# Performance work log

Measured on AMD Instinct MI355X. Metric: run time of the kernel, lower is better.

Reference implementation:

```python
import jax, jax.numpy as jnp
import numpy as np

D_MODEL = 1024
N_HEADS = 16
HEAD_DIM = D_MODEL // N_HEADS
SCALE = HEAD_DIM ** -0.5
MASK_FILL = -10000.0


def setup_inputs() -> dict:
    key = jax.random.key(0)
    ks = jax.random.split(key, 12)
    B, L, D = 2, 2048, D_MODEL
    inv = 1.0 / np.sqrt(D)
    inp = {
        "query": jax.random.normal(ks[0], (B, L, D), jnp.float32),
        "key": jax.random.normal(ks[1], (B, L, D), jnp.float32),
        "value": jax.random.normal(ks[2], (B, L, D), jnp.float32),
        "Wq": jax.random.normal(ks[3], (D, D), jnp.float32) * inv,
        "bq": jnp.zeros((D,), jnp.float32),
        "Wk": jax.random.normal(ks[4], (D, D), jnp.float32) * inv,
        "bk": jnp.zeros((D,), jnp.float32),
        "Wv": jax.random.normal(ks[5], (D, D), jnp.float32) * inv,
        "bv": jnp.zeros((D,), jnp.float32),
        "Wo": jax.random.normal(ks[6], (D, D), jnp.float32) * inv,
        "bo": jnp.zeros((D,), jnp.float32),
        "valid_mask": jax.random.randint(ks[7], (B, L), 0, 2).astype(jnp.bool_),
    }
    return inp


def reference(query, key, value, Wq, bq, Wk, bk, Wv, bv, Wo, bo, valid_mask):
    B, Lq, D = query.shape
    Lk = key.shape[1]
    H, HD = N_HEADS, HEAD_DIM
    # torch.nn.Linear: y = x @ W.T + b
    Q = (query @ Wq.T + bq).reshape(B, Lq, H, HD).transpose(0, 2, 1, 3)  # [B,H,Lq,HD]
    K = (key @ Wk.T + bk).reshape(B, Lk, H, HD).transpose(0, 2, 1, 3)    # [B,H,Lk,HD]
    V = (value @ Wv.T + bv).reshape(B, Lk, H, HD).transpose(0, 2, 1, 3)  # [B,H,Lk,HD]
    scores = jnp.einsum("bhqd,bhkd->bhqk", Q, K) * SCALE
    scores = jnp.where(valid_mask[:, None, None, :], scores, MASK_FILL)
    weights = jax.nn.softmax(scores, axis=-1)  # dropout is identity at inference
    out = jnp.einsum("bhqk,bhkd->bhqd", weights, V)
    out = out.transpose(0, 2, 1, 3).reshape(B, Lq, D)
    out = out @ Wo.T + bo
    # zero rows of fully-invalid batches
    gate = jnp.any(valid_mask, axis=1).astype(out.dtype)[:, None, None]
    return out * gate
```

## Files before the change

kernel.cpp:

```cpp
#include <hip/hip_runtime.h>
#include <hip/hip_bf16.h>

typedef __hip_bfloat16 bf16;
typedef __attribute__((ext_vector_type(8))) short s8v;
typedef __attribute__((ext_vector_type(4))) float f4v;

#define LOG2E 1.44269504088896340736f
#define CSCALE (0.125f * LOG2E)
#define MASK_B2 (-14426.950408889634f)
#define NEG_BIG (-30000.0f)

#define BB 2
#define LL 2048
#define DD 1024
#define HH 16
#define HD 64
#define MTOT 4096
#define PER_T 4194304

struct alignas(8) B4 { bf16 v[4]; };

__device__ __forceinline__ void async_cp16(const bf16* g, bf16* l) {
    __builtin_amdgcn_global_load_lds(
        (const __attribute__((address_space(1))) void*)g,
        (__attribute__((address_space(3))) void*)l, 16, 0, 0);
}

struct CvtArgs {
    const float* src[7];
    bf16* dst[7];
    int n[7];
};

__global__ __launch_bounds__(256) void cvt_kernel(CvtArgs args) {
    const int which = blockIdx.y;
    const float* __restrict__ src = args.src[which];
    bf16* __restrict__ dst = args.dst[which];
    const int n4 = args.n[which] >> 2;
    const int stride = gridDim.x * 256;
    for (int i = blockIdx.x * 256 + threadIdx.x; i < n4; i += stride) {
        const float4 f = ((const float4*)src)[i];
        B4 o;
        o.v[0] = __float2bfloat16(f.x);
        o.v[1] = __float2bfloat16(f.y);
        o.v[2] = __float2bfloat16(f.z);
        o.v[3] = __float2bfloat16(f.w);
        ((B4*)dst)[i] = o;
    }
}

struct QkvArgs {
    const bf16* A[3];
    const bf16* W[3];
    const float* bias[3];
    bf16* out[3];
};

template <int FUSED, int SWAP>
__device__ __forceinline__ void gemm_body(const bf16* __restrict__ A,
                                          const bf16* __restrict__ W,
                                          const float* __restrict__ bias,
                                          bf16* __restrict__ out_bf,
                                          float* __restrict__ out_f,
                                          float gatef, char* smem) {
    bf16* sA = (bf16*)smem;
    bf16* sB = (bf16*)(smem + 128 * 64 * 2);
    bf16* sE = (bf16*)smem;

    const int lane = threadIdx.x & 63;
    const int w = threadIdx.x >> 6;
    const int lr = lane & 15;
    const int quad = lane >> 4;
    const int wr = w >> 1, wc = w & 1;
    const int rbase = blockIdx.x * 128;
    const int cbase = blockIdx.y * 128;
    const int dma_r = lane >> 3;
    const int dma_cc = ((lane & 7) ^ dma_r) * 8;

    f4v acc[4][4] = {};
    for (int kt = 0; kt < DD / 64; kt++) {
        const int k0 = kt * 64;
        __syncthreads();
#pragma unroll
        for (int t = 0; t < 4; t++) {
            const int g = w * 4 + t;
            async_cp16(A + (size_t)(rbase + g * 8 + dma_r) * DD + k0 + dma_cc,
                       &sA[g * 512]);
            async_cp16(W + (size_t)(cbase + g * 8 + dma_r) * DD + k0 + dma_cc,
                       &sB[g * 512]);
        }
        __syncthreads();
#pragma unroll
        for (int s = 0; s < 2; s++) {
            s8v a[4], b[4];
#pragma unroll
            for (int i = 0; i < 4; i++) {
                const int row = wr * 64 + i * 16 + lr;
                a[i] = *(const s8v*)&sA[row * 64 + (((s * 4 + quad) ^ (row & 7)) * 8)];
            }
#pragma unroll
            for (int j = 0; j < 4; j++) {
                const int row = wc * 64 + j * 16 + lr;
                b[j] = *(const s8v*)&sB[row * 64 + (((s * 4 + quad) ^ (row & 7)) * 8)];
            }
#pragma unroll
            for (int i = 0; i < 4; i++)
#pragma unroll
                for (int j = 0; j < 4; j++)
                    acc[i][j] = SWAP
                        ? __builtin_amdgcn_mfma_f32_16x16x32_bf16(b[j], a[i], acc[i][j], 0, 0, 0)
                        : __builtin_amdgcn_mfma_f32_16x16x32_bf16(a[i], b[j], acc[i][j], 0, 0, 0);
        }
    }
    __syncthreads();

    if (FUSED == 0) {
#pragma unroll
        for (int j = 0; j < 4; j++) {
            const int n = cbase + wc * 64 + j * 16 + quad * 4;
            const f4v bv = *(const f4v*)&bias[n];
#pragma unroll
            for (int i = 0; i < 4; i++) {
                const int m = rbase + wr * 64 + i * 16 + lr;
                float4 o;
                o.x = (acc[i][j][0] + bv[0]) * gatef;
                o.y = (acc[i][j][1] + bv[1]) * gatef;
                o.z = (acc[i][j][2] + bv[2]) * gatef;
                o.w = (acc[i][j][3] + bv[3]) * gatef;
                *(float4*)&out_f[(size_t)m * DD + n] = o;
            }
        }
        return;
    }

    if (SWAP) {
#pragma unroll
        for (int j = 0; j < 4; j++) {
            const int n_loc = wc * 64 + j * 16 + quad * 4;
            const f4v bv = *(const f4v*)&bias[cbase + n_loc];
#pragma unroll
            for (int i = 0; i < 4; i++) {
                const int m_loc = wr * 64 + i * 16 + lr;
                B4 pk;
                pk.v[0] = __float2bfloat16(acc[i][j][0] + bv[0]);
                pk.v[1] = __float2bfloat16(acc[i][j][1] + bv[1]);
                pk.v[2] = __float2bfloat16(acc[i][j][2] + bv[2]);
                pk.v[3] = __float2bfloat16(acc[i][j][3] + bv[3]);
                *(B4*)&sE[m_loc * 136 + n_loc] = pk;
            }
        }
        __syncthreads();
        const int tid = threadIdx.x;
        const int mr_ = tid >> 4;
        const int n0 = (tid & 15) * 8;
#pragma unroll
        for (int ro = 0; ro < 8; ro++) {
            const int m_loc = ro * 16 + mr_;
            const s8v vv = *(const s8v*)&sE[m_loc * 136 + n0];
            const int m = rbase + m_loc;
            const int n = cbase + n0;
            const int b_ = m >> 11, l = m & (LL - 1);
            const int h = n >> 6, hd = n & 63;
            *(s8v*)&out_bf[(((size_t)(b_ * HH + h)) * LL + l) * HD + hd] = vv;
        }
    } else {
#pragma unroll
        for (int j = 0; j < 4; j++) {
            const int n_loc = wc * 64 + j * 16 + lr;
            const float bv = bias[cbase + n_loc];
#pragma unroll
            for (int i = 0; i < 4; i++) {
                const int m0 = wr * 64 + i * 16 + quad * 4;
                B4 pk;
                pk.v[0] = __float2bfloat16(acc[i][j][0] + bv);
                pk.v[1] = __float2bfloat16(acc[i][j][1] + bv);
                pk.v[2] = __float2bfloat16(acc[i][j][2] + bv);
                pk.v[3] = __float2bfloat16(acc[i][j][3] + bv);
                *(B4*)&sE[n_loc * 136 + m0] = pk;
            }
        }
        __syncthreads();
        const int tid = threadIdx.x;
#pragma unroll
        for (int ro = 0; ro < 8; ro++) {
            const int n_loc = ro * 16 + (tid >> 4);
            const int m0 = (tid & 15) * 8;
            const s8v vv = *(const s8v*)&sE[n_loc * 136 + m0];
            const int n = cbase + n_loc;
            const int m = rbase + m0;
            const int b_ = m >> 11, l = m & (LL - 1);
            const int h = n >> 6, hd = n & 63;
            *(s8v*)&out_bf[(((size_t)(b_ * HH + h)) * HD + hd) * LL + l] = vv;
        }
    }
}

template <int FUSED>
__global__ __launch_bounds__(256) void gemm128(QkvArgs qa,
                                               const bf16* __restrict__ Ao,
                                               const bf16* __restrict__ Wo_,
                                               const float* __restrict__ bo_,
                                               float* __restrict__ out_f,
                                               const int* __restrict__ mask) {
    __shared__ __align__(16) char smem[128 * 136 * 2];
    __shared__ int sgate;

    float gatef = 1.0f;
    if (!FUSED) {
        if (threadIdx.x == 0) sgate = 0;
        __syncthreads();
        const int b_ = (int)(blockIdx.x * 128) >> 11;
        int any = 0;
        for (int i = threadIdx.x; i < LL; i += 256) any |= mask[b_ * LL + i];
        if (any) sgate = 1;
        __syncthreads();
        gatef = sgate ? 1.0f : 0.0f;
    }

    if (FUSED) {
        const int which = blockIdx.z;
        if (which != 2)
            gemm_body<1, 1>(qa.A[which], qa.W[which], qa.bias[which],
                            qa.out[which], nullptr, 1.0f, smem);
        else
            gemm_body<1, 0>(qa.A[2], qa.W[2], qa.bias[2],
                            qa.out[2], nullptr, 1.0f, smem);
    } else {
        gemm_body<0, 1>(Ao, Wo_, bo_, nullptr, out_f, gatef, smem);
    }
}

__global__ __launch_bounds__(512) void attn_kernel(const bf16* __restrict__ Q,
                                                   const bf16* __restrict__ K,
                                                   const bf16* __restrict__ Vt,
                                                   const int* __restrict__ mask,
                                                   bf16* __restrict__ Aout) {
    __shared__ bf16 sK[2][64 * 64];
    __shared__ bf16 sV[2][64 * 64];
    __shared__ bf16 sP[8][16 * 72];
    __shared__ float sBias[LL];

    const int lane = threadIdx.x & 63;
    const int w = threadIdx.x >> 6;
    const int lr = lane & 15;
    const int quad = lane >> 4;

    const int bid = blockIdx.x;
    const int qb = bid & 15;
    const int h = (bid >> 4) & 15;
    const int b = bid >> 8;

    const size_t head_off = ((size_t)(b * HH + h)) * LL * HD;
    const bf16* Qh = Q + head_off;
    const bf16* Kh = K + head_off;
    const bf16* Vh = Vt + head_off;
    const int q0 = qb * 128 + w * 16;

    const int dma_r = lane >> 3;
    const int dma_cc = ((lane & 7) ^ dma_r) * 8;
    const int sw = lr & 7;

    {
        const int* mb = mask + b * LL;
        for (int i = threadIdx.x; i < LL; i += 512)
            sBias[i] = mb[i] ? 0.0f : MASK_B2;
        async_cp16(Kh + (size_t)(w * 8 + dma_r) * HD + dma_cc, &sK[0][w * 512]);
        async_cp16(Vh + (size_t)(w * 8 + dma_r) * LL + dma_cc, &sV[0][w * 512]);
    }
    __syncthreads();

    const s8v aq0 = *(const s8v*)(Qh + (size_t)(q0 + lr) * HD + quad * 8);
    const s8v aq1 = *(const s8v*)(Qh + (size_t)(q0 + lr) * HD + 32 + quad * 8);

    bf16* sPw = &sP[w][0];
    f4v O[4] = {};
    float mrun = NEG_BIG, lrun = 0.0f;

    int asrc[4];
#pragma unroll
    for (int r = 0; r < 4; r++) asrc[r] = (lane & 48) | (quad * 4 + r);

    for (int kt = 0; kt < LL / 64; kt++) {
        const int kbase = kt * 64;
        const bf16* kb = &sK[kt & 1][0];
        const bf16* vb = &sV[kt & 1][0];

        if (kt < LL / 64 - 1) {
            const int nb = (kt + 1) & 1;
            async_cp16(Kh + (size_t)(kbase + 64 + w * 8 + dma_r) * HD + dma_cc,
                       &sK[nb][w * 512]);
            async_cp16(Vh + (size_t)(w * 8 + dma_r) * LL + kbase + 64 + dma_cc,
                       &sV[nb][w * 512]);
        }

        f4v T[4];
#pragma unroll
        for (int j = 0; j < 4; j++) {
            const int row = 16 * j + lr;
            const s8v kb0 = *(const s8v*)&kb[row * 64 + ((quad ^ sw) * 8)];
            const s8v kb1 = *(const s8v*)&kb[row * 64 + (((quad + 4) ^ sw) * 8)];
            f4v t = {};
            t = __builtin_amdgcn_mfma_f32_16x16x32_bf16(kb0, aq0, t, 0, 0, 0);
            T[j] = __builtin_amdgcn_mfma_f32_16x16x32_bf16(kb1, aq1, t, 0, 0, 0);
        }

        s8v v0[4], v1[4];
#pragma unroll
        for (int dt = 0; dt < 4; dt++) {
            const int vrow = dt * 16 + lr;
            v0[dt] = *(const s8v*)&vb[vrow * 64 + ((quad ^ sw) * 8)];
            v1[dt] = *(const s8v*)&vb[vrow * 64 + (((quad + 4) ^ sw) * 8)];
        }

        float mloc = NEG_BIG;
#pragma unroll
        for (int j = 0; j < 4; j++) {
            const f4v bj = *(const f4v*)&sBias[kbase + j * 16 + quad * 4];
#pragma unroll
            for (int r = 0; r < 4; r++) {
                T[j][r] = T[j][r] * CSCALE + bj[r];
                mloc = fmaxf(mloc, T[j][r]);
            }
        }
        mloc = fmaxf(mloc, __shfl_xor(mloc, 16));
        mloc = fmaxf(mloc, __shfl_xor(mloc, 32));

        if (__any(mloc > mrun)) {
            const float mnew = fmaxf(mrun, mloc);
            const float alphaq = exp2f(mrun - mnew);
            mrun = mnew;
            lrun *= alphaq;
            float aB[4];
#pragma unroll
            for (int r = 0; r < 4; r++) aB[r] = __shfl(alphaq, asrc[r]);
#pragma unroll
            for (int dt = 0; dt < 4; dt++)
#pragma unroll
                for (int r = 0; r < 4; r++) O[dt][r] *= aB[r];
        }

        float ls = 0.0f;
#pragma unroll
        for (int j = 0; j < 4; j++)
#pragma unroll
            for (int r = 0; r < 4; r++) {
                const float e = exp2f(T[j][r] - mrun);
                T[j][r] = e;
                ls += e;
            }
        ls += __shfl_xor(ls, 16);
        ls += __shfl_xor(ls, 32);
        lrun += ls;

        asm volatile("" ::: "memory");
#pragma unroll
        for (int j = 0; j < 4; j++) {
            B4 pk;
            pk.v[0] = __float2bfloat16(T[j][0]);
            pk.v[1] = __float2bfloat16(T[j][1]);
            pk.v[2] = __float2bfloat16(T[j][2]);
            pk.v[3] = __float2bfloat16(T[j][3]);
            *(B4*)&sPw[lr * 72 + j * 16 + quad * 4] = pk;
        }
        asm volatile("s_waitcnt lgkmcnt(0)" ::: "memory");
        const s8v pa0 = *(const s8v*)(sPw + lr * 72 + quad * 8);
        const s8v pa1 = *(const s8v*)(sPw + lr * 72 + 32 + quad * 8);

#pragma unroll
        for (int dt = 0; dt < 4; dt++) {
            O[dt] = __builtin_amdgcn_mfma_f32_16x16x32_bf16(pa0, v0[dt], O[dt], 0, 0, 0);
            O[dt] = __builtin_amdgcn_mfma_f32_16x16x32_bf16(pa1, v1[dt], O[dt], 0, 0, 0);
        }

        __syncthreads();
    }

    const float linv = 1.0f / lrun;
    float lB[4];
#pragma unroll
    for (int r = 0; r < 4; r++) lB[r] = __shfl(linv, asrc[r]);
#pragma unroll
    for (int dt = 0; dt < 4; dt++)
#pragma unroll
        for (int r = 0; r < 4; r++) {
            const int q = q0 + quad * 4 + r;
            Aout[((size_t)(b * LL + q)) * DD + h * HD + dt * 16 + lr] =
                __float2bfloat16(O[dt][r] * lB[r]);
        }
}

extern "C" void kernel_launch(void* const* d_in, const int* in_sizes, int n_in,
                              void* d_out, int out_size, void* d_ws, size_t ws_size,
                              hipStream_t stream) {
    const float* query = (const float*)d_in[0];
    const float* key   = (const float*)d_in[1];
    const float* value = (const float*)d_in[2];
    const float* Wq = (const float*)d_in[3];
    const float* bq = (const float*)d_in[4];
    const float* Wk = (const float*)d_in[5];
    const float* bk = (const float*)d_in[6];
    const float* Wv = (const float*)d_in[7];
    const float* bv = (const float*)d_in[8];
    const float* Wo = (const float*)d_in[9];
    const float* bo = (const float*)d_in[10];
    const int* mask = (const int*)d_in[11];

    bf16* base = (bf16*)d_ws;
    bf16* qx = base;
    bf16* kx = qx + PER_T;
    bf16* vx = kx + PER_T;
    bf16* wq = vx + PER_T;
    bf16* wk = wq + DD * DD;
    bf16* wv = wk + DD * DD;
    bf16* wo = wv + DD * DD;
    bf16* Qs = wo + DD * DD;
    bf16* Ks = Qs + PER_T;
    bf16* Vst = Ks + PER_T;
    bf16* aws = Vst + PER_T;

    CvtArgs ca;
    ca.src[0] = query; ca.dst[0] = qx; ca.n[0] = PER_T;
    ca.src[1] = key;   ca.dst[1] = kx; ca.n[1] = PER_T;
    ca.src[2] = value; ca.dst[2] = vx; ca.n[2] = PER_T;
    ca.src[3] = Wq;    ca.dst[3] = wq; ca.n[3] = DD * DD;
    ca.src[4] = Wk;    ca.dst[4] = wk; ca.n[4] = DD * DD;
    ca.src[5] = Wv;    ca.dst[5] = wv; ca.n[5] = DD * DD;
    ca.src[6] = Wo;    ca.dst[6] = wo; ca.n[6] = DD * DD;
    cvt_kernel<<<dim3(1024, 7), 256, 0, stream>>>(ca);

    QkvArgs qa;
    qa.A[0] = qx; qa.W[0] = wq; qa.bias[0] = bq; qa.out[0] = Qs;
    qa.A[1] = kx; qa.W[1] = wk; qa.bias[1] = bk; qa.out[1] = Ks;
    qa.A[2] = vx; qa.W[2] = wv; qa.bias[2] = bv; qa.out[2] = Vst;

    gemm128<1><<<dim3(MTOT / 128, DD / 128, 3), 256, 0, stream>>>(
        qa, nullptr, nullptr, nullptr, nullptr, nullptr);

    attn_kernel<<<BB * HH * (LL / 128), 512, 0, stream>>>(Qs, Ks, Vst, mask, aws);

    QkvArgs dummy{};
    gemm128<0><<<dim3(MTOT / 128, DD / 128, 1), 256, 0, stream>>>(
        dummy, aws, wo, bo, (float*)d_out, mask);
}
```

Baseline: 258.1 us.

## Keep softmax probabilities in registers by transposing PV MFMA and permuting K rows

```diff
diff --git a/kernel.cpp b/kernel.cpp
--- a/kernel.cpp
+++ b/kernel.cpp
@@ -237,7 +237,6 @@
                                                    bf16* __restrict__ Aout) {
     __shared__ bf16 sK[2][64 * 64];
     __shared__ bf16 sV[2][64 * 64];
-    __shared__ bf16 sP[8][16 * 72];
     __shared__ float sBias[LL];
 
     const int lane = threadIdx.x & 63;
@@ -257,28 +256,27 @@
     const int q0 = qb * 128 + w * 16;
 
     const int dma_r = lane >> 3;
-    const int dma_cc = ((lane & 7) ^ dma_r) * 8;
-    const int sw = lr & 7;
+    const int dma_cv = ((lane & 7) ^ dma_r) * 8;
+    const int dma_ck = ((lane & 7) ^ ((dma_r & 3) | ((w & 1) << 2))) * 8;
 
     {
         const int* mb = mask + b * LL;
         for (int i = threadIdx.x; i < LL; i += 512)
             sBias[i] = mb[i] ? 0.0f : MASK_B2;
-        async_cp16(Kh + (size_t)(w * 8 + dma_r) * HD + dma_cc, &sK[0][w * 512]);
-        async_cp16(Vh + (size_t)(w * 8 + dma_r) * LL + dma_cc, &sV[0][w * 512]);
+        async_cp16(Kh + (size_t)(w * 8 + dma_r) * HD + dma_ck, &sK[0][w * 512]);
+        async_cp16(Vh + (size_t)(w * 8 + dma_r) * LL + dma_cv, &sV[0][w * 512]);
     }
     __syncthreads();
 
     const s8v aq0 = *(const s8v*)(Qh + (size_t)(q0 + lr) * HD + quad * 8);
     const s8v aq1 = *(const s8v*)(Qh + (size_t)(q0 + lr) * HD + 32 + quad * 8);
 
-    bf16* sPw = &sP[w][0];
     f4v O[4] = {};
     float mrun = NEG_BIG, lrun = 0.0f;
 
-    int asrc[4];
-#pragma unroll
-    for (int r = 0; r < 4; r++) asrc[r] = (lane & 48) | (quad * 4 + r);
+    const int swk = (lr & 3) | (((lr >> 2) & 1) << 2);
+    const int swv = lr & 7;
+    const int krow0 = 8 * (lr >> 2) + (lr & 3);
 
     for (int kt = 0; kt < LL / 64; kt++) {
         const int kbase = kt * 64;
@@ -287,18 +285,18 @@
 
         if (kt < LL / 64 - 1) {
             const int nb = (kt + 1) & 1;
-            async_cp16(Kh + (size_t)(kbase + 64 + w * 8 + dma_r) * HD + dma_cc,
+            async_cp16(Kh + (size_t)(kbase + 64 + w * 8 + dma_r) * HD + dma_ck,
                        &sK[nb][w * 512]);
-            async_cp16(Vh + (size_t)(w * 8 + dma_r) * LL + kbase + 64 + dma_cc,
+            async_cp16(Vh + (size_t)(w * 8 + dma_r) * LL + kbase + 64 + dma_cv,
                        &sV[nb][w * 512]);
         }
 
         f4v T[4];
 #pragma unroll
         for (int j = 0; j < 4; j++) {
-            const int row = 16 * j + lr;
-            const s8v kb0 = *(const s8v*)&kb[row * 64 + ((quad ^ sw) * 8)];
-            const s8v kb1 = *(const s8v*)&kb[row * 64 + (((quad + 4) ^ sw) * 8)];
+            const int row = krow0 + 32 * (j >> 1) + 4 * (j & 1);
+            const s8v kb0 = *(const s8v*)&kb[row * 64 + ((quad ^ swk) * 8)];
+            const s8v kb1 = *(const s8v*)&kb[row * 64 + (((quad + 4) ^ swk) * 8)];
             f4v t = {};
             t = __builtin_amdgcn_mfma_f32_16x16x32_bf16(kb0, aq0, t, 0, 0, 0);
             T[j] = __builtin_amdgcn_mfma_f32_16x16x32_bf16(kb1, aq1, t, 0, 0, 0);
@@ -308,14 +306,14 @@
 #pragma unroll
         for (int dt = 0; dt < 4; dt++) {
             const int vrow = dt * 16 + lr;
-            v0[dt] = *(const s8v*)&vb[vrow * 64 + ((quad ^ sw) * 8)];
-            v1[dt] = *(const s8v*)&vb[vrow * 64 + (((quad + 4) ^ sw) * 8)];
+            v0[dt] = *(const s8v*)&vb[vrow * 64 + ((quad ^ swv) * 8)];
+            v1[dt] = *(const s8v*)&vb[vrow * 64 + (((quad + 4) ^ swv) * 8)];
         }
 
         float mloc = NEG_BIG;
 #pragma unroll
         for (int j = 0; j < 4; j++) {
-            const f4v bj = *(const f4v*)&sBias[kbase + j * 16 + quad * 4];
+            const f4v bj = *(const f4v*)&sBias[kbase + 32 * (j >> 1) + 8 * quad + 4 * (j & 1)];
 #pragma unroll
             for (int r = 0; r < 4; r++) {
                 T[j][r] = T[j][r] * CSCALE + bj[r];
@@ -330,13 +328,10 @@
             const float alphaq = exp2f(mrun - mnew);
             mrun = mnew;
             lrun *= alphaq;
-            float aB[4];
-#pragma unroll
-            for (int r = 0; r < 4; r++) aB[r] = __shfl(alphaq, asrc[r]);
 #pragma unroll
             for (int dt = 0; dt < 4; dt++)
 #pragma unroll
-                for (int r = 0; r < 4; r++) O[dt][r] *= aB[r];
+                for (int r = 0; r < 4; r++) O[dt][r] *= alphaq;
         }
 
         float ls = 0.0f;
@@ -352,41 +347,32 @@
         ls += __shfl_xor(ls, 32);
         lrun += ls;
 
-        asm volatile("" ::: "memory");
-#pragma unroll
-        for (int j = 0; j < 4; j++) {
-            B4 pk;
-            pk.v[0] = __float2bfloat16(T[j][0]);
-            pk.v[1] = __float2bfloat16(T[j][1]);
-            pk.v[2] = __float2bfloat16(T[j][2]);
-            pk.v[3] = __float2bfloat16(T[j][3]);
-            *(B4*)&sPw[lr * 72 + j * 16 + quad * 4] = pk;
-        }
-        asm volatile("s_waitcnt lgkmcnt(0)" ::: "memory");
-        const s8v pa0 = *(const s8v*)(sPw + lr * 72 + quad * 8);
-        const s8v pa1 = *(const s8v*)(sPw + lr * 72 + 32 + quad * 8);
+        union { s8v v; bf16 e[8]; } p0, p1;
+#pragma unroll
+        for (int r = 0; r < 4; r++) {
+            p0.e[r]     = __float2bfloat16(T[0][r]);
+            p0.e[r + 4] = __float2bfloat16(T[1][r]);
+            p1.e[r]     = __float2bfloat16(T[2][r]);
+            p1.e[r + 4] = __float2bfloat16(T[3][r]);
+        }
 
 #pragma unroll
         for (int dt = 0; dt < 4; dt++) {
-            O[dt] = __builtin_amdgcn_mfma_f32_16x16x32_bf16(pa0, v0[dt], O[dt], 0, 0, 0);
-            O[dt] = __builtin_amdgcn_mfma_f32_16x16x32_bf16(pa1, v1[dt], O[dt], 0, 0, 0);
+            O[dt] = __builtin_amdgcn_mfma_f32_16x16x32_bf16(v0[dt], p0.v, O[dt], 0, 0, 0);
+            O[dt] = __builtin_amdgcn_mfma_f32_16x16x32_bf16(v1[dt], p1.v, O[dt], 0, 0, 0);
         }
 
         __syncthreads();
     }
 
     const float linv = 1.0f / lrun;
-    float lB[4];
-#pragma unroll
-    for (int r = 0; r < 4; r++) lB[r] = __shfl(linv, asrc[r]);
-#pragma unroll
-    for (int dt = 0; dt < 4; dt++)
-#pragma unroll
-        for (int r = 0; r < 4; r++) {
-            const int q = q0 + quad * 4 + r;
-            Aout[((size_t)(b * LL + q)) * DD + h * HD + dt * 16 + lr] =
-                __float2bfloat16(O[dt][r] * lB[r]);
-        }
+#pragma unroll
+    for (int dt = 0; dt < 4; dt++) {
+        B4 o;
+#pragma unroll
+        for (int r = 0; r < 4; r++) o.v[r] = __float2bfloat16(O[dt][r] * linv);
+        *(B4*)&Aout[((size_t)(b * LL + q0 + lr)) * DD + h * HD + dt * 16 + quad * 4] = o;
+    }
 }
 
 extern "C" void kernel_launch(void* const* d_in, const int* in_sizes, int n_in,
```

New measurement: 254.6 us. About the same (-1.4%).
